# Kernel tuning notes

Measured on AMD Instinct MI355X. Metric: run time of the kernel, lower is better.

The kernel has to match this reference:

```python
import jax, jax.numpy as jnp
import numpy as np

IN_FEATURES = 256
OUT_FEATURES = 128
ALPHA = 0.2  # LeakyReLU negative slope
NEG_INF = -9e15
N_NODES = 8192


def _xavier_uniform(key, shape, gain):
    fan_in, fan_out = shape[0], shape[1]
    limit = gain * np.sqrt(6.0 / (fan_in + fan_out))
    return jax.random.uniform(key, shape, jnp.float32, -limit, limit)


def setup_inputs() -> dict:
    key = jax.random.key(0)
    k_h, k_adj, k_W, k_a = jax.random.split(key, 4)
    h = jax.random.normal(k_h, (N_NODES, IN_FEATURES), dtype=jnp.float32)
    adj = jax.random.randint(k_adj, (N_NODES, N_NODES), 0, 2, dtype=jnp.int32)
    W = _xavier_uniform(k_W, (IN_FEATURES, OUT_FEATURES), gain=1.414)
    a = _xavier_uniform(k_a, (2 * OUT_FEATURES, 1), gain=1.414)
    return {"h": h, "adj": adj, "W": W, "a": a}


def reference(h, adj, W, a):
    # Wh: (N, F_out)
    Wh = h @ W
    # Decompose a = [a1; a2]; e_ij = leakyrelu(Wh_i . a1 + Wh_j . a2)
    # == the original concat([Wh_i, Wh_j]) @ a, without the O(N^2*2F) tensor.
    a1 = a[:OUT_FEATURES, 0]  # (F_out,)
    a2 = a[OUT_FEATURES:, 0]  # (F_out,)
    src = Wh @ a1  # (N,)
    dst = Wh @ a2  # (N,)
    e = jax.nn.leaky_relu(src[:, None] + dst[None, :], negative_slope=ALPHA)  # (N, N)
    attention = jnp.where(adj > 0, e, NEG_INF)
    attention = jax.nn.softmax(attention, axis=1)
    # dropout p=0.0 (eval) -> identity
    h_prime = attention @ Wh  # (N, F_out)
    return jax.nn.elu(h_prime)  # concat=True
```

## Files before the change

kernel.cpp:

```cpp
#include <hip/hip_runtime.h>

#define N_NODES 8192
#define IN_F    256
#define OUT_F   128
#define ALPHA_S 0.2f

typedef __attribute__((ext_vector_type(8))) short  short8;
typedef __attribute__((ext_vector_type(4))) short  short4v;
typedef __attribute__((ext_vector_type(4))) float  floatx4;
typedef __attribute__((ext_vector_type(4))) int    intx4;
typedef __attribute__((ext_vector_type(4))) float  fx4;

static __device__ __forceinline__ short f2bf(float f) {
    union { float f; unsigned int i; } u; u.f = f;
    unsigned int r = u.i + 0x7FFFu + ((u.i >> 16) & 1u);
    return (short)(r >> 16);
}

__global__ __launch_bounds__(512) void k_wh(
    const float* __restrict__ h,
    const float* __restrict__ W,
    const float* __restrict__ a,
    short* __restrict__ WhT,
    float* __restrict__ src,
    float* __restrict__ dst)
{
    __shared__ short Wt[OUT_F][IN_F + 8];
    __shared__ short htile[32][IN_F + 8];
    __shared__ float q1s[IN_F], q2s[IN_F];
    __shared__ short wh_t[OUT_F][40];

    const int t      = threadIdx.x;
    const int lane   = t & 63;
    const int wave   = t >> 6;
    const int r_base = blockIdx.x * 32;

#pragma unroll
    for (int rep = 0; rep < 4; ++rep) {
        const int idx = rep * 8192 + t * 16;
        const int k   = idx >> 7;
        const int f   = idx & 127;
        fx4 w0 = *(const fx4*)(W + idx);
        fx4 w1 = *(const fx4*)(W + idx + 4);
        fx4 w2 = *(const fx4*)(W + idx + 8);
        fx4 w3 = *(const fx4*)(W + idx + 12);
        fx4 a10 = *(const fx4*)(a + f);
        fx4 a11 = *(const fx4*)(a + f + 4);
        fx4 a12 = *(const fx4*)(a + f + 8);
        fx4 a13 = *(const fx4*)(a + f + 12);
        fx4 a20 = *(const fx4*)(a + OUT_F + f);
        fx4 a21 = *(const fx4*)(a + OUT_F + f + 4);
        fx4 a22 = *(const fx4*)(a + OUT_F + f + 8);
        fx4 a23 = *(const fx4*)(a + OUT_F + f + 12);
        float p1 = 0.f, p2 = 0.f;
#pragma unroll
        for (int e = 0; e < 4; ++e) {
            p1 = fmaf(w0[e], a10[e], p1); p2 = fmaf(w0[e], a20[e], p2);
            p1 = fmaf(w1[e], a11[e], p1); p2 = fmaf(w1[e], a21[e], p2);
            p1 = fmaf(w2[e], a12[e], p1); p2 = fmaf(w2[e], a22[e], p2);
            p1 = fmaf(w3[e], a13[e], p1); p2 = fmaf(w3[e], a23[e], p2);
        }
#pragma unroll
        for (int e = 0; e < 4; ++e) {
            Wt[f + e][k]      = f2bf(w0[e]);
            Wt[f + 4 + e][k]  = f2bf(w1[e]);
            Wt[f + 8 + e][k]  = f2bf(w2[e]);
            Wt[f + 12 + e][k] = f2bf(w3[e]);
        }
#pragma unroll
        for (int m = 1; m < 8; m <<= 1) {
            p1 += __shfl_xor(p1, m, 64);
            p2 += __shfl_xor(p2, m, 64);
        }
        if ((t & 7) == 0) { q1s[k] = p1; q2s[k] = p2; }
    }

    const int r0   = t >> 4;
    const int fgrp = t & 15;
    const int k0   = fgrp * 16;
    fx4 h0, h1, h2, h3;
    {
        const float* hp = h + (size_t)(r_base + r0) * IN_F + k0;
        h0 = *(const fx4*)hp; h1 = *(const fx4*)(hp + 4);
        h2 = *(const fx4*)(hp + 8); h3 = *(const fx4*)(hp + 12);
        short8 b0, b1;
#pragma unroll
        for (int e = 0; e < 4; ++e) {
            b0[e]     = f2bf(h0[e]); b0[4 + e] = f2bf(h1[e]);
            b1[e]     = f2bf(h2[e]); b1[4 + e] = f2bf(h3[e]);
        }
        *(short8*)&htile[r0][k0]     = b0;
        *(short8*)&htile[r0][k0 + 8] = b1;
    }
    __syncthreads();

    {
        float sp = 0.f, dp = 0.f;
#pragma unroll
        for (int e = 0; e < 4; ++e) {
            sp = fmaf(h0[e], q1s[k0 + e], sp);      dp = fmaf(h0[e], q2s[k0 + e], dp);
            sp = fmaf(h1[e], q1s[k0 + 4 + e], sp);  dp = fmaf(h1[e], q2s[k0 + 4 + e], dp);
            sp = fmaf(h2[e], q1s[k0 + 8 + e], sp);  dp = fmaf(h2[e], q2s[k0 + 8 + e], dp);
            sp = fmaf(h3[e], q1s[k0 + 12 + e], sp); dp = fmaf(h3[e], q2s[k0 + 12 + e], dp);
        }
#pragma unroll
        for (int m = 1; m < 16; m <<= 1) {
            sp += __shfl_xor(sp, m, 64);
            dp += __shfl_xor(dp, m, 64);
        }
        if (fgrp == 0) { src[r_base + r0] = sp; dst[r_base + r0] = dp; }
    }

    const int ln15 = lane & 15;
    const int q    = lane >> 4;
    const int f0   = wave * 16;
    floatx4 c0 = {0.f, 0.f, 0.f, 0.f};
    floatx4 c1 = {0.f, 0.f, 0.f, 0.f};
#pragma unroll
    for (int s = 0; s < 8; ++s) {
        short8 bf  = *(const short8*)&Wt[f0 + ln15][s * 32 + q * 8];
        short8 a0f = *(const short8*)&htile[ln15][s * 32 + q * 8];
        short8 a1f = *(const short8*)&htile[16 + ln15][s * 32 + q * 8];
        c0 = __builtin_amdgcn_mfma_f32_16x16x32_bf16(a0f, bf, c0, 0, 0, 0);
        c1 = __builtin_amdgcn_mfma_f32_16x16x32_bf16(a1f, bf, c1, 0, 0, 0);
    }
    {
        short4v p0, p1;
#pragma unroll
        for (int r = 0; r < 4; ++r) { p0[r] = f2bf(c0[r]); p1[r] = f2bf(c1[r]); }
        *(short4v*)&wh_t[f0 + ln15][q * 4]      = p0;
        *(short4v*)&wh_t[f0 + ln15][16 + q * 4] = p1;
    }
    __syncthreads();
    {
        const int f    = t >> 2;
        const int half = t & 3;
        *(short8*)(WhT + (size_t)f * N_NODES + r_base + half * 8) =
            *(const short8*)&wh_t[f][half * 8];
    }
}

#define BM 32
#define BK 128
#define WPAD (BK + 8)
#define JCH 2048
#define NIT2 (JCH / BK)

__global__ __launch_bounds__(512, 4) void k_attn(
    const int*   __restrict__ adj,
    const short* __restrict__ WhT,
    const float* __restrict__ src,
    const float* __restrict__ dstv,
    float* __restrict__ numer_part,
    float* __restrict__ denom_part)
{
    __shared__ short wbuf[2][BM * WPAD];

    const int t    = threadIdx.x;
    const int lane = t & 63;
    const int wave = t >> 6;
    const int rg   = blockIdx.x >> 2;
    const int jc   = blockIdx.x & 3;
    const int r0   = rg * BM;
    const int jb   = jc * JCH;

    const int sm  = t >> 4;
    const int sk0 = (t & 15) * 8;
    const float srow = src[r0 + sm];
    const int*   abase = adj  + (size_t)(r0 + sm) * N_NODES + jb + sk0;
    const float* dbase = dstv + jb + sk0;

    const int ln15 = lane & 15;
    const int q    = lane >> 4;
    const int f0   = wave * 16;
    const short* bbase = WhT + (size_t)(f0 + ln15) * N_NODES + jb + q * 8;

    floatx4 acc0 = {0.f, 0.f, 0.f, 0.f};
    floatx4 acc1 = {0.f, 0.f, 0.f, 0.f};
    floatx4 dac0 = {0.f, 0.f, 0.f, 0.f};
    floatx4 dac1 = {0.f, 0.f, 0.f, 0.f};
    short8 ones;
#pragma unroll
    for (int j = 0; j < 8; ++j) ones[j] = (short)0x3F80;

    intx4 m0 = *(const intx4*)abase;
    intx4 m1 = *(const intx4*)(abase + 4);
    fx4   d0 = *(const fx4*)dbase;
    fx4   d1 = *(const fx4*)(dbase + 4);

    for (int it = 0; it < NIT2; ++it) {
        const int p = it & 1;
        short8 wv;
#pragma unroll
        for (int e = 0; e < 4; ++e) {
            float x = srow + d0[e];
            float l = fmaxf(x, ALPHA_S * x);
            wv[e] = (m0[e] > 0) ? f2bf(__expf(l)) : (short)0;
        }
#pragma unroll
        for (int e = 0; e < 4; ++e) {
            float x = srow + d1[e];
            float l = fmaxf(x, ALPHA_S * x);
            wv[4 + e] = (m1[e] > 0) ? f2bf(__expf(l)) : (short)0;
        }
        *(short8*)&wbuf[p][sm * WPAD + sk0] = wv;
        if (it + 1 < NIT2) {
            const int o = (it + 1) * BK;
            m0 = *(const intx4*)(abase + o);
            m1 = *(const intx4*)(abase + o + 4);
            d0 = *(const fx4*)(dbase + o);
            d1 = *(const fx4*)(dbase + o + 4);
        }
        __syncthreads();
        const short* ab = &wbuf[p][ln15 * WPAD + q * 8];
        const short* bb = bbase + it * BK;
#pragma unroll
        for (int ks = 0; ks < 4; ++ks) {
            short8 afr0 = *(const short8*)(ab + ks * 32);
            short8 afr1 = *(const short8*)(ab + 16 * WPAD + ks * 32);
            short8 bfr  = *(const short8*)(bb + ks * 32);
            acc0 = __builtin_amdgcn_mfma_f32_16x16x32_bf16(afr0, bfr, acc0, 0, 0, 0);
            acc1 = __builtin_amdgcn_mfma_f32_16x16x32_bf16(afr1, bfr, acc1, 0, 0, 0);
            if (wave == 0) {
                dac0 = __builtin_amdgcn_mfma_f32_16x16x32_bf16(afr0, ones, dac0, 0, 0, 0);
                dac1 = __builtin_amdgcn_mfma_f32_16x16x32_bf16(afr1, ones, dac1, 0, 0, 0);
            }
        }
    }

    float* np = numer_part + ((size_t)jc * N_NODES + r0) * OUT_F;
#pragma unroll
    for (int r = 0; r < 4; ++r) {
        np[(size_t)(q * 4 + r) * OUT_F + f0 + ln15]      = acc0[r];
        np[(size_t)(16 + q * 4 + r) * OUT_F + f0 + ln15] = acc1[r];
    }
    if (wave == 0 && ln15 == 0) {
        float* dp = denom_part + (size_t)jc * N_NODES + r0;
#pragma unroll
        for (int r = 0; r < 4; ++r) {
            dp[q * 4 + r]      = dac0[r];
            dp[16 + q * 4 + r] = dac1[r];
        }
    }
}

__global__ void k_final(const float* __restrict__ numer_part,
                        const float* __restrict__ denom_part,
                        float* __restrict__ out) {
    const int idx = blockIdx.x * 256 + threadIdx.x;
    const int row = idx >> 7;
    float v  = 0.f, dn = 0.f;
#pragma unroll
    for (int jc = 0; jc < 4; ++jc) {
        v  += numer_part[(size_t)jc * N_NODES * OUT_F + idx];
        dn += denom_part[(size_t)jc * N_NODES + row];
    }
    v = (dn != 0.f) ? (v / dn) : 0.f;
    v = v > 0.f ? v : (__expf(v) - 1.f);
    out[idx] = v;
}

extern "C" void kernel_launch(void* const* d_in, const int* in_sizes, int n_in,
                              void* d_out, int out_size, void* d_ws, size_t ws_size,
                              hipStream_t stream) {
    const float* h   = (const float*)d_in[0];
    const int*   adj = (const int*)d_in[1];
    const float* W   = (const float*)d_in[2];
    const float* a   = (const float*)d_in[3];
    float* out = (float*)d_out;

    char*  ws    = (char*)d_ws;
    float* denom_part = (float*)ws;
    short* WhT        = (short*)(ws + (128 << 10));
    float* src        = (float*)(ws + (128 << 10) + (2 << 20));
    float* dst        = src + N_NODES;
    float* numer_part = (float*)(ws + (4 << 20));

    k_wh   <<<256, 512, 0, stream>>>(h, W, a, WhT, src, dst);
    k_attn <<<1024, 512, 0, stream>>>(adj, WhT, src, dst, numer_part, denom_part);
    k_final<<<4096, 256, 0, stream>>>(numer_part, denom_part, out);
}
```

Baseline: 406.0 us.

## Restructure attention kernel so each wave owns 16 rows without LDS staging

The attention kernel is reorganized so each wave computes exp-weights for its own 16 rows directly in registers, in the MFMA A-fragment layout. This removes the shared-memory buffer and the per-iteration __syncthreads. Each wave now accumulates all 128 output features across 8 accumulator tiles and computes its own denominator via an MFMA against ones. The j-dimension split is raised from 4 to 8, with 256-thread blocks, and the final reduction and workspace offsets are adjusted to match. In exchange, each wave re-reads WhT from global/L2 with no sharing across waves, register pressure rises, and the partial-sum buffers double in size.

```diff
diff --git a/kernel.cpp b/kernel.cpp
--- a/kernel.cpp
+++ b/kernel.cpp
@@ -140,13 +140,12 @@
     }
 }
 
-#define BM 32
-#define BK 128
-#define WPAD (BK + 8)
-#define JCH 2048
-#define NIT2 (JCH / BK)
-
-__global__ __launch_bounds__(512, 4) void k_attn(
+#define JSPLIT 8
+#define JCH    (N_NODES / JSPLIT)
+#define SJ     64
+#define NSTEP  (JCH / SJ)
+
+__global__ __launch_bounds__(256, 4) void k_attn(
     const int*   __restrict__ adj,
     const short* __restrict__ WhT,
     const float* __restrict__ src,
@@ -154,93 +153,87 @@
     float* __restrict__ numer_part,
     float* __restrict__ denom_part)
 {
-    __shared__ short wbuf[2][BM * WPAD];
-
     const int t    = threadIdx.x;
     const int lane = t & 63;
     const int wave = t >> 6;
-    const int rg   = blockIdx.x >> 2;
-    const int jc   = blockIdx.x & 3;
-    const int r0   = rg * BM;
+    const int rg   = blockIdx.x >> 3;
+    const int jc   = blockIdx.x & 7;
+    const int r0w  = rg * 64 + wave * 16;
     const int jb   = jc * JCH;
-
-    const int sm  = t >> 4;
-    const int sk0 = (t & 15) * 8;
-    const float srow = src[r0 + sm];
-    const int*   abase = adj  + (size_t)(r0 + sm) * N_NODES + jb + sk0;
-    const float* dbase = dstv + jb + sk0;
 
     const int ln15 = lane & 15;
     const int q    = lane >> 4;
-    const int f0   = wave * 16;
-    const short* bbase = WhT + (size_t)(f0 + ln15) * N_NODES + jb + q * 8;
-
-    floatx4 acc0 = {0.f, 0.f, 0.f, 0.f};
-    floatx4 acc1 = {0.f, 0.f, 0.f, 0.f};
-    floatx4 dac0 = {0.f, 0.f, 0.f, 0.f};
-    floatx4 dac1 = {0.f, 0.f, 0.f, 0.f};
+
+    const float srow = src[r0w + ln15];
+    const int*   ab = adj  + (size_t)(r0w + ln15) * N_NODES + jb + q * 8;
+    const float* db = dstv + jb + q * 8;
+    const short* bb = WhT + (size_t)ln15 * N_NODES + jb + q * 8;
+
+    floatx4 acc[8];
+#pragma unroll
+    for (int ft = 0; ft < 8; ++ft) acc[ft] = (floatx4){0.f, 0.f, 0.f, 0.f};
+    floatx4 dacc = {0.f, 0.f, 0.f, 0.f};
     short8 ones;
 #pragma unroll
     for (int j = 0; j < 8; ++j) ones[j] = (short)0x3F80;
 
-    intx4 m0 = *(const intx4*)abase;
-    intx4 m1 = *(const intx4*)(abase + 4);
-    fx4   d0 = *(const fx4*)dbase;
-    fx4   d1 = *(const fx4*)(dbase + 4);
-
-    for (int it = 0; it < NIT2; ++it) {
-        const int p = it & 1;
-        short8 wv;
-#pragma unroll
-        for (int e = 0; e < 4; ++e) {
-            float x = srow + d0[e];
-            float l = fmaxf(x, ALPHA_S * x);
-            wv[e] = (m0[e] > 0) ? f2bf(__expf(l)) : (short)0;
-        }
-#pragma unroll
-        for (int e = 0; e < 4; ++e) {
-            float x = srow + d1[e];
-            float l = fmaxf(x, ALPHA_S * x);
-            wv[4 + e] = (m1[e] > 0) ? f2bf(__expf(l)) : (short)0;
-        }
-        *(short8*)&wbuf[p][sm * WPAD + sk0] = wv;
-        if (it + 1 < NIT2) {
-            const int o = (it + 1) * BK;
-            m0 = *(const intx4*)(abase + o);
-            m1 = *(const intx4*)(abase + o + 4);
-            d0 = *(const fx4*)(dbase + o);
-            d1 = *(const fx4*)(dbase + o + 4);
-        }
-        __syncthreads();
-        const short* ab = &wbuf[p][ln15 * WPAD + q * 8];
-        const short* bb = bbase + it * BK;
-#pragma unroll
-        for (int ks = 0; ks < 4; ++ks) {
-            short8 afr0 = *(const short8*)(ab + ks * 32);
-            short8 afr1 = *(const short8*)(ab + 16 * WPAD + ks * 32);
-            short8 bfr  = *(const short8*)(bb + ks * 32);
-            acc0 = __builtin_amdgcn_mfma_f32_16x16x32_bf16(afr0, bfr, acc0, 0, 0, 0);
-            acc1 = __builtin_amdgcn_mfma_f32_16x16x32_bf16(afr1, bfr, acc1, 0, 0, 0);
-            if (wave == 0) {
-                dac0 = __builtin_amdgcn_mfma_f32_16x16x32_bf16(afr0, ones, dac0, 0, 0, 0);
-                dac1 = __builtin_amdgcn_mfma_f32_16x16x32_bf16(afr1, ones, dac1, 0, 0, 0);
-            }
-        }
-    }
-
-    float* np = numer_part + ((size_t)jc * N_NODES + r0) * OUT_F;
-#pragma unroll
-    for (int r = 0; r < 4; ++r) {
-        np[(size_t)(q * 4 + r) * OUT_F + f0 + ln15]      = acc0[r];
-        np[(size_t)(16 + q * 4 + r) * OUT_F + f0 + ln15] = acc1[r];
-    }
-    if (wave == 0 && ln15 == 0) {
-        float* dp = denom_part + (size_t)jc * N_NODES + r0;
-#pragma unroll
-        for (int r = 0; r < 4; ++r) {
-            dp[q * 4 + r]      = dac0[r];
-            dp[16 + q * 4 + r] = dac1[r];
-        }
+    intx4 m0 = *(const intx4*)(ab);
+    intx4 m1 = *(const intx4*)(ab + 4);
+    intx4 m2 = *(const intx4*)(ab + 32);
+    intx4 m3 = *(const intx4*)(ab + 36);
+
+    for (int s = 0; s < NSTEP; ++s) {
+        const int off = s * SJ;
+        intx4 c0 = m0, c1 = m1, c2 = m2, c3 = m3;
+        if (s + 1 < NSTEP) {
+            const int o2 = off + SJ;
+            m0 = *(const intx4*)(ab + o2);
+            m1 = *(const intx4*)(ab + o2 + 4);
+            m2 = *(const intx4*)(ab + o2 + 32);
+            m3 = *(const intx4*)(ab + o2 + 36);
+        }
+        fx4 d0 = *(const fx4*)(db + off);
+        fx4 d1 = *(const fx4*)(db + off + 4);
+        fx4 d2 = *(const fx4*)(db + off + 32);
+        fx4 d3 = *(const fx4*)(db + off + 36);
+
+        short8 A0, A1;
+#pragma unroll
+        for (int e = 0; e < 4; ++e) {
+            float x, l;
+            x = srow + d0[e]; l = fmaxf(x, ALPHA_S * x);
+            A0[e]     = (c0[e] > 0) ? f2bf(__expf(l)) : (short)0;
+            x = srow + d1[e]; l = fmaxf(x, ALPHA_S * x);
+            A0[4 + e] = (c1[e] > 0) ? f2bf(__expf(l)) : (short)0;
+            x = srow + d2[e]; l = fmaxf(x, ALPHA_S * x);
+            A1[e]     = (c2[e] > 0) ? f2bf(__expf(l)) : (short)0;
+            x = srow + d3[e]; l = fmaxf(x, ALPHA_S * x);
+            A1[4 + e] = (c3[e] > 0) ? f2bf(__expf(l)) : (short)0;
+        }
+
+        dacc = __builtin_amdgcn_mfma_f32_16x16x32_bf16(A0, ones, dacc, 0, 0, 0);
+        dacc = __builtin_amdgcn_mfma_f32_16x16x32_bf16(A1, ones, dacc, 0, 0, 0);
+
+#pragma unroll
+        for (int ft = 0; ft < 8; ++ft) {
+            const short* bp = bb + (size_t)ft * 16 * N_NODES + off;
+            short8 B0 = *(const short8*)bp;
+            short8 B1 = *(const short8*)(bp + 32);
+            acc[ft] = __builtin_amdgcn_mfma_f32_16x16x32_bf16(A0, B0, acc[ft], 0, 0, 0);
+            acc[ft] = __builtin_amdgcn_mfma_f32_16x16x32_bf16(A1, B1, acc[ft], 0, 0, 0);
+        }
+    }
+
+    float* np = numer_part + ((size_t)jc * N_NODES + r0w) * OUT_F;
+#pragma unroll
+    for (int ft = 0; ft < 8; ++ft)
+#pragma unroll
+        for (int r = 0; r < 4; ++r)
+            np[(size_t)(q * 4 + r) * OUT_F + ft * 16 + ln15] = acc[ft][r];
+    if (ln15 == 0) {
+        float* dp = denom_part + (size_t)jc * N_NODES + r0w;
+#pragma unroll
+        for (int r = 0; r < 4; ++r) dp[q * 4 + r] = dacc[r];
     }
 }
 
@@ -249,9 +242,9 @@
                         float* __restrict__ out) {
     const int idx = blockIdx.x * 256 + threadIdx.x;
     const int row = idx >> 7;
-    float v  = 0.f, dn = 0.f;
-#pragma unroll
-    for (int jc = 0; jc < 4; ++jc) {
+    float v = 0.f, dn = 0.f;
+#pragma unroll
+    for (int jc = 0; jc < JSPLIT; ++jc) {
         v  += numer_part[(size_t)jc * N_NODES * OUT_F + idx];
         dn += denom_part[(size_t)jc * N_NODES + row];
     }
@@ -269,14 +262,14 @@
     const float* a   = (const float*)d_in[3];
     float* out = (float*)d_out;
 
-    char*  ws    = (char*)d_ws;
+    char*  ws         = (char*)d_ws;
     float* denom_part = (float*)ws;
-    short* WhT        = (short*)(ws + (128 << 10));
-    float* src        = (float*)(ws + (128 << 10) + (2 << 20));
+    short* WhT        = (short*)(ws + (256 << 10));
+    float* src        = (float*)(ws + (256 << 10) + (2 << 20));
     float* dst        = src + N_NODES;
     float* numer_part = (float*)(ws + (4 << 20));
 
     k_wh   <<<256, 512, 0, stream>>>(h, W, a, WhT, src, dst);
-    k_attn <<<1024, 512, 0, stream>>>(adj, WhT, src, dst, numer_part, denom_part);
+    k_attn <<<1024, 256, 0, stream>>>(adj, WhT, src, dst, numer_part, denom_part);
     k_final<<<4096, 256, 0, stream>>>(numer_part, denom_part, out);
 }
```

Result: slower. 470.7 us (+15.9%).
